# Kernel optimization log

Measured on AMD Instinct MI355X. Metric: run time of the kernel, lower is better.

The kernel has to match this reference:

```python
import jax, jax.numpy as jnp
import numpy as np

BATCH = 32
NUM_PIXELS = 3072
NUM_NEURONS = 4096
NUM_STEPS = 100
DT = 0.001
TAU = 0.03
ETA = DT / TAU  # eta = dt / tau, per load_params


def setup_inputs() -> dict:
    key = jax.random.key(0)
    k1, k2 = jax.random.split(key)
    x = jax.random.normal(k1, (BATCH, NUM_PIXELS), dtype=jnp.float32)
    phi = jax.random.normal(k2, (NUM_PIXELS, NUM_NEURONS), dtype=jnp.float32) * 0.5
    # l2-normalize dictionary columns (norm_weights behavior, keeps dynamics stable)
    phi = phi / jnp.linalg.norm(phi, axis=0, keepdims=True)
    sparse_mult = jnp.float32(0.1)
    return {"x": x, "phi": phi, "sparse_mult": sparse_mult}


def _soft_threshold(u, lam):
    # non-rectified soft threshold: shrink toward zero by lam
    return jnp.where(u > lam, u - lam,
                     jnp.where(u < -lam, u + lam, jnp.zeros_like(u)))


def reference(x, phi, sparse_mult):
    # excitatory drive b: [batch, neurons]
    b = x @ phi
    # lateral inhibition g = phi^T phi - I: [neurons, neurons]
    n = phi.shape[1]
    g = phi.T @ phi - jnp.eye(n, dtype=phi.dtype)

    u0 = jnp.zeros_like(b)
    a0 = _soft_threshold(u0, sparse_mult)  # zeros

    def step(carry, _):
        u, a = carry
        du = b - a @ g - u
        u_new = u + ETA * du
        a_new = _soft_threshold(u_new, sparse_mult)
        return (u_new, a_new), None

    # infer_coefficients runs num_steps - 1 update iterations
    (u_final, a_final), _ = jax.lax.scan(step, (u0, a0), None, length=NUM_STEPS - 1)
    return a_final
```

## Files before the change

### kernel.cpp

```cpp
#include <hip/hip_runtime.h>

#define BATCH 32
#define PIX   3072
#define NEU   4096
#define STEPS 99
#define ETA   (0.001f / 0.03f)
#define NBLK  256
#define TPB   512
#define SLOT  (BATCH * NEU)

typedef __bf16 bf16x8 __attribute__((ext_vector_type(8)));
typedef float  f32x4  __attribute__((ext_vector_type(4)));

__device__ __forceinline__ float softt(float u, float lam) {
    return u > lam ? u - lam : (u < -lam ? u + lam : 0.0f);
}

__device__ __forceinline__ unsigned short f2b(float f) {
    unsigned int u = __builtin_bit_cast(unsigned int, f);
    u = (u + 0x7FFFu + ((u >> 16) & 1u)) >> 16;
    return (unsigned short)u;
}

__device__ __forceinline__ bf16x8 ldfrag_g(const unsigned short* p) {
    uint4 v = *(const uint4*)p;
    return __builtin_bit_cast(bf16x8, v);
}

__global__ void transp(const float* __restrict__ phi, unsigned short* __restrict__ phiT) {
    __shared__ float t[64][65];
    const int n0 = blockIdx.x * 64, p0 = blockIdx.y * 64;
    const int tid = threadIdx.x;
    #pragma unroll
    for (int pass = 0; pass < 4; ++pass) {
        const int r  = pass * 16 + (tid >> 4);
        const int c4 = (tid & 15) * 4;
        float4 v = *(const float4*)(phi + (size_t)(p0 + r) * NEU + n0 + c4);
        t[r][c4 + 0] = v.x; t[r][c4 + 1] = v.y; t[r][c4 + 2] = v.z; t[r][c4 + 3] = v.w;
    }
    __syncthreads();
    #pragma unroll
    for (int pass = 0; pass < 2; ++pass) {
        const int cp = pass * 32 + (tid >> 3);
        const int p8 = (tid & 7) * 8;
        unsigned int w0 = (unsigned int)f2b(t[p8 + 0][cp]) | ((unsigned int)f2b(t[p8 + 1][cp]) << 16);
        unsigned int w1 = (unsigned int)f2b(t[p8 + 2][cp]) | ((unsigned int)f2b(t[p8 + 3][cp]) << 16);
        unsigned int w2 = (unsigned int)f2b(t[p8 + 4][cp]) | ((unsigned int)f2b(t[p8 + 5][cp]) << 16);
        unsigned int w3 = (unsigned int)f2b(t[p8 + 6][cp]) | ((unsigned int)f2b(t[p8 + 7][cp]) << 16);
        uint4 o = make_uint4(w0, w1, w2, w3);
        *(uint4*)(phiT + (size_t)(n0 + cp) * PIX + p0 + p8) = o;
    }
}

__global__ void gemm_G(const unsigned short* __restrict__ phiT, unsigned short* __restrict__ G) {
    if (blockIdx.y > blockIdx.x) return;
    __shared__ __align__(16) unsigned short lds[2][128 * 40];
    const int m0 = blockIdx.y * 128, n0 = blockIdx.x * 128;
    const int tid  = threadIdx.x;
    const int lane = tid & 63, w = tid >> 6;
    const int wm = (w & 1) * 64, wn = (w >> 1) * 64;
    const int q8 = (lane >> 4) * 8, l15 = lane & 15;
    f32x4 acc[4][4] = {};
    for (int k0 = 0; k0 < PIX; k0 += 32) {
        __syncthreads();
        #pragma unroll
        for (int it = 0; it < 2; ++it) {
            const int id = tid + 256 * it;
            const int row = id >> 2, q = id & 3;
            uint4 va = *(const uint4*)(phiT + (size_t)(m0 + row) * PIX + k0 + q * 8);
            *(uint4*)(&lds[0][row * 40 + q * 8]) = va;
            uint4 vb = *(const uint4*)(phiT + (size_t)(n0 + row) * PIX + k0 + q * 8);
            *(uint4*)(&lds[1][row * 40 + q * 8]) = vb;
        }
        __syncthreads();
        bf16x8 af[4], bfr[4];
        #pragma unroll
        for (int i = 0; i < 4; ++i) {
            af[i]  = *(const bf16x8*)(&lds[0][(wm + i * 16 + l15) * 40 + q8]);
            bfr[i] = *(const bf16x8*)(&lds[1][(wn + i * 16 + l15) * 40 + q8]);
        }
        #pragma unroll
        for (int i = 0; i < 4; ++i)
            #pragma unroll
            for (int j = 0; j < 4; ++j)
                acc[i][j] = __builtin_amdgcn_mfma_f32_16x16x32_bf16(af[i], bfr[j], acc[i][j], 0, 0, 0);
    }
    const int q = lane >> 4;
    const bool offdiag = (blockIdx.y != blockIdx.x);
    #pragma unroll
    for (int i = 0; i < 4; ++i)
        #pragma unroll
        for (int j = 0; j < 4; ++j) {
            unsigned short pk[4];
            #pragma unroll
            for (int r = 0; r < 4; ++r) {
                const int gm = m0 + wm + i * 16 + q * 4 + r;
                const int gn = n0 + wn + j * 16 + l15;
                const unsigned short v = f2b(acc[i][j][r]);
                G[(size_t)gm * NEU + gn] = v;
                pk[r] = v;
            }
            if (offdiag) {
                const int gm0 = m0 + wm + i * 16 + q * 4;
                const int gn  = n0 + wn + j * 16 + l15;
                *(ushort4*)(G + (size_t)gn * NEU + gm0) = make_ushort4(pk[0], pk[1], pk[2], pk[3]);
            }
        }
}

__global__ void lca_binit(const float* __restrict__ x, const unsigned short* __restrict__ phiT,
                          float* __restrict__ b, unsigned int* __restrict__ arr) {
    __shared__ float red[8 * 512];
    const int tid = threadIdx.x;
    const int lane = tid & 63, w = tid >> 6;
    const int n0 = blockIdx.x * 16;
    const int kbase = w * (PIX / 8);
    const int q8 = (lane >> 4) * 8, l15 = lane & 15;
    if (blockIdx.x < NBLK && tid < 16) arr[blockIdx.x * 16 + tid] = 0u;
    f32x4 acc[2] = {};
    const unsigned short* Brow = phiT + (size_t)(n0 + l15) * PIX + kbase + q8;
    const float* X0 = x + (size_t)l15 * PIX + kbase + q8;
    const float* X1 = x + (size_t)(16 + l15) * PIX + kbase + q8;
    #pragma unroll 4
    for (int kk = 0; kk < PIX / 8; kk += 32) {
        bf16x8 bg = ldfrag_g(Brow + kk);
        float4 xa0 = *(const float4*)(X0 + kk), xb0 = *(const float4*)(X0 + kk + 4);
        float4 xa1 = *(const float4*)(X1 + kk), xb1 = *(const float4*)(X1 + kk + 4);
        bf16x8 a0, a1;
        a0[0]=(__bf16)xa0.x; a0[1]=(__bf16)xa0.y; a0[2]=(__bf16)xa0.z; a0[3]=(__bf16)xa0.w;
        a0[4]=(__bf16)xb0.x; a0[5]=(__bf16)xb0.y; a0[6]=(__bf16)xb0.z; a0[7]=(__bf16)xb0.w;
        a1[0]=(__bf16)xa1.x; a1[1]=(__bf16)xa1.y; a1[2]=(__bf16)xa1.z; a1[3]=(__bf16)xa1.w;
        a1[4]=(__bf16)xb1.x; a1[5]=(__bf16)xb1.y; a1[6]=(__bf16)xb1.z; a1[7]=(__bf16)xb1.w;
        acc[0] = __builtin_amdgcn_mfma_f32_16x16x32_bf16(a0, bg, acc[0], 0, 0, 0);
        acc[1] = __builtin_amdgcn_mfma_f32_16x16x32_bf16(a1, bg, acc[1], 0, 0, 0);
    }
    const int q = lane >> 4;
    #pragma unroll
    for (int mt = 0; mt < 2; ++mt)
        #pragma unroll
        for (int r = 0; r < 4; ++r)
            red[w * 512 + (mt * 16 + q * 4 + r) * 16 + l15] = acc[mt][r];
    __syncthreads();
    float s = 0.f;
    #pragma unroll
    for (int w8 = 0; w8 < 8; ++w8) s += red[w8 * 512 + tid];
    const int m = tid >> 4, n = n0 + (tid & 15);
    b[(size_t)m * NEU + n] = s;
}

__device__ __forceinline__ void publish16(unsigned short* slot, size_t idx,
                                          float av, int lane) {
    unsigned int v  = f2b(av);
    unsigned int d0 = v | ((unsigned int)__shfl_xor((int)v, 1, 64) << 16);
    unsigned int hi = (unsigned int)__shfl_xor((int)d0, 2, 64);
    if ((lane & 3) == 0) {
        unsigned long long val = (unsigned long long)d0 | ((unsigned long long)hi << 32);
        __hip_atomic_store((unsigned long long*)slot + (idx >> 2), val,
                           __ATOMIC_RELAXED, __HIP_MEMORY_SCOPE_AGENT);
    }
}

__device__ __forceinline__ void setflag(unsigned int* arr, unsigned int e,
                                        int tid, int bx) {
    __syncthreads();
    if (tid == 0)
        __hip_atomic_store(arr + bx * 16, e, __ATOMIC_RELAXED, __HIP_MEMORY_SCOPE_AGENT);
}

__global__ void __launch_bounds__(TPB, 2)
lca_persist(const unsigned short* __restrict__ G, const float* __restrict__ b,
            unsigned short* __restrict__ rot, float* __restrict__ aout,
            const float* __restrict__ lamp, unsigned int* __restrict__ arr) {
    __shared__ float red[8 * 512];
    const int tid  = threadIdx.x;
    const int lane = tid & 63, w = tid >> 6;
    const int l15  = lane & 15, q = lane >> 4;
    const int q8   = q * 8;
    const int c    = blockIdx.x & 127;
    const int h    = blockIdx.x >> 7;
    const int n0   = c * 32;
    const int rb   = h * 16;
    const int kbase = w * (NEU / 8);
    const int pbase = h * 128 + w * 16;

    bf16x8 gf[2][16];
    #pragma unroll
    for (int j = 0; j < 2; ++j)
        #pragma unroll
        for (int f = 0; f < 16; ++f)
            gf[j][f] = ldfrag_g(G + (size_t)(n0 + j * 16 + l15) * NEU + kbase + f * 32 + q8);

    const int m0i = tid >> 5, nn0 = tid & 31;
    const size_t idx0 = (size_t)(rb + m0i) * NEU + n0 + nn0;
    const float bv0 = b[idx0];
    const float lam = lamp[0];

    float uv0 = ETA * bv0;
    float av0 = softt(uv0, lam);

    const size_t aoff0 = (size_t)(rb + l15) * NEU + kbase + q8;

    publish16(rot, idx0, av0, lane);
    setflag(arr, 1u, tid, blockIdx.x);

    for (int step = 1; step < STEPS; ++step) {
        const unsigned short* A = rot + (size_t)(step - 1) * SLOT;

        {
            const unsigned int* fp = arr + (size_t)(pbase + l15) * 16;
            for (;;) {
                unsigned int v = __hip_atomic_load(fp, __ATOMIC_RELAXED,
                                                   __HIP_MEMORY_SCOPE_AGENT);
                if (__ballot(v < (unsigned int)step) == 0ULL) break;
            }
            asm volatile("" : "+s"(A));
        }

        f32x4 acc00 = {}, acc01 = {};
        #pragma unroll
        for (int hb = 0; hb < 2; ++hb) {
            bf16x8 s0[8];
            #pragma unroll
            for (int f = 0; f < 8; ++f)
                s0[f] = ldfrag_g(A + aoff0 + (hb * 8 + f) * 32);
            #pragma unroll
            for (int f = 0; f < 8; ++f) {
                const int g = hb * 8 + f;
                acc00 = __builtin_amdgcn_mfma_f32_16x16x32_bf16(s0[f], gf[0][g], acc00, 0, 0, 0);
                acc01 = __builtin_amdgcn_mfma_f32_16x16x32_bf16(s0[f], gf[1][g], acc01, 0, 0, 0);
            }
        }
        #pragma unroll
        for (int r = 0; r < 4; ++r) {
            red[w * 512 + (q * 4 + r) * 32 + l15]      = acc00[r];
            red[w * 512 + (q * 4 + r) * 32 + 16 + l15] = acc01[r];
        }
        __syncthreads();
        float s0v = 0.f;
        #pragma unroll
        for (int w8 = 0; w8 < 8; ++w8) s0v += red[w8 * 512 + tid];

        uv0 = fmaf(ETA, bv0 - s0v + av0 - uv0, uv0);
        av0 = softt(uv0, lam);

        if (step == STEPS - 1) {
            aout[idx0] = av0;
        } else {
            publish16(rot + (size_t)step * SLOT, idx0, av0, lane);
            setflag(arr, (unsigned int)(step + 1), tid, blockIdx.x);
        }
    }
}

__global__ void lca_init_f(const float* __restrict__ x, const float* __restrict__ phi,
                           float* __restrict__ b, float* __restrict__ u,
                           float* __restrict__ a) {
    const int n  = blockIdx.x * 64 + (threadIdx.x & 63);
    const int bi = blockIdx.y * 4 + (threadIdx.x >> 6);
    const float* xr = x + bi * PIX;
    float acc = 0.f;
    #pragma unroll 4
    for (int p = 0; p < PIX; ++p) acc = fmaf(xr[p], phi[p * NEU + n], acc);
    const int idx = bi * NEU + n;
    b[idx] = acc; u[idx] = 0.f; a[idx] = 0.f;
}
__global__ void lca_s_f(const float* __restrict__ a, const float* __restrict__ phi,
                        float* __restrict__ s) {
    const int lane = threadIdx.x & 63, w = threadIdx.x >> 6;
    const int bi = blockIdx.y, p0 = (blockIdx.x * 4 + w) * 8;
    const float* ar = a + bi * NEU;
    float acc[8] = {};
    for (int i = 0; i < NEU / 64; ++i) {
        const int n = i * 64 + lane;
        const float av = ar[n];
        #pragma unroll
        for (int j = 0; j < 8; ++j) acc[j] = fmaf(av, phi[(p0 + j) * NEU + n], acc[j]);
    }
    float out = 0.f;
    #pragma unroll
    for (int j = 0; j < 8; ++j) {
        float v = acc[j];
        v += __shfl_xor(v, 1, 64); v += __shfl_xor(v, 2, 64); v += __shfl_xor(v, 4, 64);
        v += __shfl_xor(v, 8, 64); v += __shfl_xor(v, 16, 64); v += __shfl_xor(v, 32, 64);
        if (lane == j) out = v;
    }
    if (lane < 8) s[bi * PIX + p0 + lane] = out;
}
__global__ void lca_t_f(const float* __restrict__ s, const float* __restrict__ phi,
                        const float* __restrict__ b, float* __restrict__ u,
                        float* __restrict__ a, const float* __restrict__ lamp) {
    __shared__ float ls[8 * 256];
    const int n = blockIdx.x * 64 + (threadIdx.x & 63);
    const int slot = threadIdx.x >> 6;
    const int bb = blockIdx.y * 8 + slot;
    float acc = 0.f;
    for (int c = 0; c < PIX; c += 256) {
        __syncthreads();
        for (int e = threadIdx.x; e < 8 * 256; e += 512) {
            const int r = e >> 8, p = e & 255;
            ls[e] = s[(blockIdx.y * 8 + r) * PIX + c + p];
        }
        __syncthreads();
        const float* lrow = ls + slot * 256;
        #pragma unroll 8
        for (int p = 0; p < 256; ++p) acc = fmaf(lrow[p], phi[(c + p) * NEU + n], acc);
    }
    const float lam = lamp[0];
    const int idx = bb * NEU + n;
    const float uo = u[idx];
    const float du = b[idx] - acc + a[idx] - uo;
    const float un = fmaf(ETA, du, uo);
    u[idx] = un; a[idx] = softt(un, lam);
}

extern "C" void kernel_launch(void* const* d_in, const int* in_sizes, int n_in,
                              void* d_out, int out_size, void* d_ws, size_t ws_size,
                              hipStream_t stream) {
    const float* x    = (const float*)d_in[0];
    const float* phi  = (const float*)d_in[1];
    const float* lamp = (const float*)d_in[2];
    float* a = (float*)d_out;
    char* ws = (char*)d_ws;

    const size_t ROT_OFF  = 0;
    const size_t ROT_BYTES= (size_t)(STEPS - 1) * SLOT * 2;
    const size_t PHIT_OFF = 0;
    const size_t G_OFF    = ROT_OFF + ROT_BYTES;
    const size_t B_OFF    = G_OFF + (size_t)NEU * NEU * 2;
    const size_t ARR_OFF  = B_OFF + (size_t)BATCH * NEU * 4;
    const size_t NEED     = ARR_OFF + (size_t)NBLK * 64;

    if (ws_size >= NEED) {
        unsigned short* phiT = (unsigned short*)(ws + PHIT_OFF);
        unsigned short* rot  = (unsigned short*)(ws + ROT_OFF);
        unsigned short* G    = (unsigned short*)(ws + G_OFF);
        float*          b    = (float*)(ws + B_OFF);
        unsigned int*   arr  = (unsigned int*)(ws + ARR_OFF);

        transp<<<dim3(NEU / 64, PIX / 64), 256, 0, stream>>>(phi, phiT);
        gemm_G<<<dim3(32, 32), 256, 0, stream>>>(phiT, G);
        lca_binit<<<256, 512, 0, stream>>>(x, phiT, b, arr);

        void* args[6];
        const unsigned short* Gc = G;
        const float* bc = b;
        const float* lc = lamp;
        args[0] = (void*)&Gc;
        args[1] = (void*)&bc;
        args[2] = (void*)&rot;
        args[3] = (void*)&a;
        args[4] = (void*)&lc;
        args[5] = (void*)&arr;
        hipLaunchCooperativeKernel((const void*)lca_persist, dim3(NBLK), dim3(TPB),
                                   args, 0, stream);
    } else {
        float* fws = (float*)d_ws;
        float* b = fws;
        float* u = fws + BATCH * NEU;
        float* s = fws + 2 * BATCH * NEU;
        lca_init_f<<<dim3(64, 8), 256, 0, stream>>>(x, phi, b, u, a);
        for (int it = 0; it < STEPS; ++it) {
            lca_s_f<<<dim3(96, 32), 256, 0, stream>>>(a, phi, s);
            lca_t_f<<<dim3(64, 4), 512, 0, stream>>>(s, phi, b, u, a, lamp);
        }
    }
}
```

Before: 819.4 us.

## Replace per-block step flags with sentinel-filled data polling in persistent LCA

Removes the per-block flag array and the barrier+flag store after each publish. Instead the rotating activation buffer is pre-filled with an all-ones sentinel, and consumers poll the data itself with agent-scope atomic loads until no 32-bit word equals the sentinel. The reduction buffer is double-buffered so the dropped end-of-step barrier does not cause a shared-memory race. The change saves a barrier and a separate flag round trip per step. In exchange it adds a fill kernel over the ~25MB rotation buffer, relies on a published value never packing to 0xFFFFFFFF, and assumes relaxed 64-bit stores are seen atomically.

New measurement: 1.509 ms. 84.1% more time.

```diff
diff --git a/kernel.cpp b/kernel.cpp
--- a/kernel.cpp
+++ b/kernel.cpp
@@ -11,6 +11,7 @@
 
 typedef __bf16 bf16x8 __attribute__((ext_vector_type(8)));
 typedef float  f32x4  __attribute__((ext_vector_type(4)));
+typedef unsigned long long u64;
 
 __device__ __forceinline__ float softt(float u, float lam) {
     return u > lam ? u - lam : (u < -lam ? u + lam : 0.0f);
@@ -109,14 +110,13 @@
 }
 
 __global__ void lca_binit(const float* __restrict__ x, const unsigned short* __restrict__ phiT,
-                          float* __restrict__ b, unsigned int* __restrict__ arr) {
+                          float* __restrict__ b) {
     __shared__ float red[8 * 512];
     const int tid = threadIdx.x;
     const int lane = tid & 63, w = tid >> 6;
     const int n0 = blockIdx.x * 16;
     const int kbase = w * (PIX / 8);
     const int q8 = (lane >> 4) * 8, l15 = lane & 15;
-    if (blockIdx.x < NBLK && tid < 16) arr[blockIdx.x * 16 + tid] = 0u;
     f32x4 acc[2] = {};
     const unsigned short* Brow = phiT + (size_t)(n0 + l15) * PIX + kbase + q8;
     const float* X0 = x + (size_t)l15 * PIX + kbase + q8;
@@ -148,30 +148,59 @@
     b[(size_t)m * NEU + n] = s;
 }
 
+__global__ void fillsent(u64* __restrict__ rot, size_t n64) {
+    size_t i = (size_t)blockIdx.x * blockDim.x + threadIdx.x;
+    const size_t stride = (size_t)gridDim.x * blockDim.x;
+    for (; i < n64; i += stride)
+        __hip_atomic_store(rot + i, ~0ULL, __ATOMIC_RELAXED, __HIP_MEMORY_SCOPE_AGENT);
+}
+
 __device__ __forceinline__ void publish16(unsigned short* slot, size_t idx,
                                           float av, int lane) {
     unsigned int v  = f2b(av);
     unsigned int d0 = v | ((unsigned int)__shfl_xor((int)v, 1, 64) << 16);
     unsigned int hi = (unsigned int)__shfl_xor((int)d0, 2, 64);
     if ((lane & 3) == 0) {
-        unsigned long long val = (unsigned long long)d0 | ((unsigned long long)hi << 32);
-        __hip_atomic_store((unsigned long long*)slot + (idx >> 2), val,
+        u64 val = (u64)d0 | ((u64)hi << 32);
+        __hip_atomic_store((u64*)slot + (idx >> 2), val,
                            __ATOMIC_RELAXED, __HIP_MEMORY_SCOPE_AGENT);
     }
 }
 
-__device__ __forceinline__ void setflag(unsigned int* arr, unsigned int e,
-                                        int tid, int bx) {
-    __syncthreads();
-    if (tid == 0)
-        __hip_atomic_store(arr + bx * 16, e, __ATOMIC_RELAXED, __HIP_MEMORY_SCOPE_AGENT);
+__device__ __forceinline__ void agent_ld16(const u64* base, u64 v[16]) {
+    #pragma unroll
+    for (int f = 0; f < 8; ++f) {
+        v[2 * f]     = __hip_atomic_load(base + f * 8,     __ATOMIC_RELAXED,
+                                         __HIP_MEMORY_SCOPE_AGENT);
+        v[2 * f + 1] = __hip_atomic_load(base + f * 8 + 1, __ATOMIC_RELAXED,
+                                         __HIP_MEMORY_SCOPE_AGENT);
+    }
+}
+__device__ __forceinline__ unsigned chk16(const u64 v[16]) {
+    unsigned bad = 0;
+    #pragma unroll
+    for (int i = 0; i < 16; ++i)
+        bad |= (unsigned)(((unsigned)v[i] == ~0u) | ((unsigned)(v[i] >> 32) == ~0u));
+    return bad;
+}
+__device__ __forceinline__ void validate16(const u64* base, u64 v[16]) {
+    unsigned bad = chk16(v);
+    while (__ballot(bad)) {
+        agent_ld16(base, v);
+        bad = chk16(v);
+    }
+}
+__device__ __forceinline__ bf16x8 frag_of(u64 lo, u64 hi) {
+    uint4 t = make_uint4((unsigned)lo, (unsigned)(lo >> 32),
+                         (unsigned)hi, (unsigned)(hi >> 32));
+    return __builtin_bit_cast(bf16x8, t);
 }
 
 __global__ void __launch_bounds__(TPB, 2)
 lca_persist(const unsigned short* __restrict__ G, const float* __restrict__ b,
             unsigned short* __restrict__ rot, float* __restrict__ aout,
-            const float* __restrict__ lamp, unsigned int* __restrict__ arr) {
-    __shared__ float red[8 * 512];
+            const float* __restrict__ lamp) {
+    __shared__ float red[2][8 * 512];
     const int tid  = threadIdx.x;
     const int lane = tid & 63, w = tid >> 6;
     const int l15  = lane & 15, q = lane >> 4;
@@ -181,7 +210,6 @@
     const int n0   = c * 32;
     const int rb   = h * 16;
     const int kbase = w * (NEU / 8);
-    const int pbase = h * 128 + w * 16;
 
     bf16x8 gf[2][16];
     #pragma unroll
@@ -199,46 +227,44 @@
     float av0 = softt(uv0, lam);
 
     const size_t aoff0 = (size_t)(rb + l15) * NEU + kbase + q8;
+    const size_t au64  = aoff0 >> 2;
 
     publish16(rot, idx0, av0, lane);
-    setflag(arr, 1u, tid, blockIdx.x);
 
     for (int step = 1; step < STEPS; ++step) {
-        const unsigned short* A = rot + (size_t)(step - 1) * SLOT;
-
-        {
-            const unsigned int* fp = arr + (size_t)(pbase + l15) * 16;
-            for (;;) {
-                unsigned int v = __hip_atomic_load(fp, __ATOMIC_RELAXED,
-                                                   __HIP_MEMORY_SCOPE_AGENT);
-                if (__ballot(v < (unsigned int)step) == 0ULL) break;
-            }
-            asm volatile("" : "+s"(A));
-        }
+        const u64* A64 = (const u64*)(rot + (size_t)(step - 1) * SLOT) + au64;
+        const int  p   = step & 1;
+
+        u64 v0[16];
+        agent_ld16(A64, v0);
 
         f32x4 acc00 = {}, acc01 = {};
-        #pragma unroll
-        for (int hb = 0; hb < 2; ++hb) {
-            bf16x8 s0[8];
-            #pragma unroll
-            for (int f = 0; f < 8; ++f)
-                s0[f] = ldfrag_g(A + aoff0 + (hb * 8 + f) * 32);
-            #pragma unroll
-            for (int f = 0; f < 8; ++f) {
-                const int g = hb * 8 + f;
-                acc00 = __builtin_amdgcn_mfma_f32_16x16x32_bf16(s0[f], gf[0][g], acc00, 0, 0, 0);
-                acc01 = __builtin_amdgcn_mfma_f32_16x16x32_bf16(s0[f], gf[1][g], acc01, 0, 0, 0);
-            }
-        }
+        validate16(A64, v0);
+        #pragma unroll
+        for (int f = 0; f < 8; ++f) {
+            bf16x8 s = frag_of(v0[2 * f], v0[2 * f + 1]);
+            acc00 = __builtin_amdgcn_mfma_f32_16x16x32_bf16(s, gf[0][f], acc00, 0, 0, 0);
+            acc01 = __builtin_amdgcn_mfma_f32_16x16x32_bf16(s, gf[1][f], acc01, 0, 0, 0);
+        }
+        u64 v1[16];
+        agent_ld16(A64 + 64, v1);
+        validate16(A64 + 64, v1);
+        #pragma unroll
+        for (int f = 0; f < 8; ++f) {
+            bf16x8 s = frag_of(v1[2 * f], v1[2 * f + 1]);
+            acc00 = __builtin_amdgcn_mfma_f32_16x16x32_bf16(s, gf[0][8 + f], acc00, 0, 0, 0);
+            acc01 = __builtin_amdgcn_mfma_f32_16x16x32_bf16(s, gf[1][8 + f], acc01, 0, 0, 0);
+        }
+
         #pragma unroll
         for (int r = 0; r < 4; ++r) {
-            red[w * 512 + (q * 4 + r) * 32 + l15]      = acc00[r];
-            red[w * 512 + (q * 4 + r) * 32 + 16 + l15] = acc01[r];
+            red[p][w * 512 + (q * 4 + r) * 32 + l15]      = acc00[r];
+            red[p][w * 512 + (q * 4 + r) * 32 + 16 + l15] = acc01[r];
         }
         __syncthreads();
         float s0v = 0.f;
         #pragma unroll
-        for (int w8 = 0; w8 < 8; ++w8) s0v += red[w8 * 512 + tid];
+        for (int w8 = 0; w8 < 8; ++w8) s0v += red[p][w8 * 512 + tid];
 
         uv0 = fmaf(ETA, bv0 - s0v + av0 - uv0, uv0);
         av0 = softt(uv0, lam);
@@ -247,7 +273,6 @@
             aout[idx0] = av0;
         } else {
             publish16(rot + (size_t)step * SLOT, idx0, av0, lane);
-            setflag(arr, (unsigned int)(step + 1), tid, blockIdx.x);
         }
     }
 }
@@ -327,21 +352,20 @@
     const size_t PHIT_OFF = 0;
     const size_t G_OFF    = ROT_OFF + ROT_BYTES;
     const size_t B_OFF    = G_OFF + (size_t)NEU * NEU * 2;
-    const size_t ARR_OFF  = B_OFF + (size_t)BATCH * NEU * 4;
-    const size_t NEED     = ARR_OFF + (size_t)NBLK * 64;
+    const size_t NEED     = B_OFF + (size_t)BATCH * NEU * 4;
 
     if (ws_size >= NEED) {
         unsigned short* phiT = (unsigned short*)(ws + PHIT_OFF);
         unsigned short* rot  = (unsigned short*)(ws + ROT_OFF);
         unsigned short* G    = (unsigned short*)(ws + G_OFF);
         float*          b    = (float*)(ws + B_OFF);
-        unsigned int*   arr  = (unsigned int*)(ws + ARR_OFF);
 
         transp<<<dim3(NEU / 64, PIX / 64), 256, 0, stream>>>(phi, phiT);
         gemm_G<<<dim3(32, 32), 256, 0, stream>>>(phiT, G);
-        lca_binit<<<256, 512, 0, stream>>>(x, phiT, b, arr);
-
-        void* args[6];
+        lca_binit<<<256, 512, 0, stream>>>(x, phiT, b);
+        fillsent<<<1024, 512, 0, stream>>>((u64*)rot, ROT_BYTES / 8);
+
+        void* args[5];
         const unsigned short* Gc = G;
         const float* bc = b;
         const float* lc = lamp;
@@ -350,7 +374,6 @@
         args[2] = (void*)&rot;
         args[3] = (void*)&a;
         args[4] = (void*)&lc;
-        args[5] = (void*)&arr;
         hipLaunchCooperativeKernel((const void*)lca_persist, dim3(NBLK), dim3(TPB),
                                    args, 0, stream);
     } else {
```
